# Kernel optimization log

Measured on AMD Instinct MI355X. Metric: run time of the kernel, lower is better.

## Reference

```python
import jax, jax.numpy as jnp
import numpy as np


def setup_inputs() -> dict:
    key = jax.random.key(0)
    k_x, k1, k2, k3 = jax.random.split(key, 4)
    dim, hidden, out_dim = 4096, 8192, 4096
    x = jax.random.normal(k_x, (4, 2048, dim), dtype=jnp.float32)
    # VNNILinear initializes weight = randn(out, in) * 0.02
    w1 = jax.random.normal(k1, (hidden, dim), dtype=jnp.float32) * 0.02
    w2 = jax.random.normal(k2, (out_dim, hidden), dtype=jnp.float32) * 0.02
    w3 = jax.random.normal(k3, (hidden, dim), dtype=jnp.float32) * 0.02
    return {"x": x, "w1": w1, "w2": w2, "w3": w3}


def _quant_linear(x, w):
    """Emulate VNNILinear int8 weight-quantized matmul (inference path).

    Per-output-channel symmetric quant: scale = max|w_row| / 127,
    w_q = round(w / scale) in int8, y = x @ (w_q * scale).T.
    """
    w_max = jnp.clip(jnp.max(jnp.abs(w), axis=1, keepdims=True), 1e-6)  # [out,1]
    scale_w = w_max / 127.0
    w_q = jnp.round(w / scale_w).astype(jnp.int8)
    w_dq = w_q.astype(jnp.float32) * scale_w  # dequantized weight
    return jnp.einsum('bsd,hd->bsh', x, w_dq)


def reference(x, w1, w2, w3):
    # SwiGLU: w2( silu(w1(x)) * w3(x) ), all bias-free, int8 VNNI weight quant
    h = jax.nn.silu(_quant_linear(x, w1)) * _quant_linear(x, w3)  # [B,S,hidden]
    return _quant_linear(h, w2)  # [B,S,out_dim]
```

## Files before the change

### kernel.cpp

```cpp
#include <hip/hip_runtime.h>
#include <hip/hip_bf16.h>
#include <stdint.h>


typedef short bf16x8 __attribute__((ext_vector_type(8)));
typedef float f32x4  __attribute__((ext_vector_type(4)));
typedef float f32x16 __attribute__((ext_vector_type(16)));
typedef int   i32x4  __attribute__((ext_vector_type(4)));
typedef int   i32x16 __attribute__((ext_vector_type(16)));

__device__ __forceinline__ unsigned short f2bf(float f) {
  unsigned u = __builtin_bit_cast(unsigned, f);
  u += 0x7FFFu + ((u >> 16) & 1u);
  return (unsigned short)(u >> 16);
}

#define GLOAD_LDS16(gaddr, laddr)                                             \
  __builtin_amdgcn_global_load_lds(                                           \
      (const __attribute__((address_space(1))) void*)(gaddr),                 \
      (__attribute__((address_space(3))) void*)(laddr), 16, 0, 0)

#define FENCE()      asm volatile("" ::: "memory")
#define BAR()        __builtin_amdgcn_s_barrier()
#define WAIT_LGKM(n) asm volatile("s_waitcnt lgkmcnt(" #n ")" ::: "memory")
#define WAIT_VM8()   asm volatile("s_waitcnt vmcnt(8)" ::: "memory")
#define WAIT_VM4()   asm volatile("s_waitcnt vmcnt(4)" ::: "memory")
#define WAIT_VM0()   asm volatile("s_waitcnt vmcnt(0)" ::: "memory")
#define SFENCE()     __builtin_amdgcn_sched_barrier(0)
#define PRIO1()      __builtin_amdgcn_s_setprio(1)
#define PRIO0()      __builtin_amdgcn_s_setprio(0)


template <int NCH>
__global__ void quant_rows_i8_sp(const float* __restrict__ w,
                                 char* __restrict__ q,
                                 float* __restrict__ scale, float clip) {
  const int cols = NCH * 1024;
  const float* wr = w + (size_t)blockIdx.x * cols;
  char* qr = q + (size_t)blockIdx.x * cols;

  float4 v[NCH];
  float m = 0.f;
#pragma unroll
  for (int j = 0; j < NCH; ++j) {
    v[j] = *reinterpret_cast<const float4*>(wr + threadIdx.x * 4 + j * 1024);
    m = fmaxf(m, fmaxf(fmaxf(fabsf(v[j].x), fabsf(v[j].y)),
                       fmaxf(fabsf(v[j].z), fabsf(v[j].w))));
  }
#pragma unroll
  for (int off = 32; off; off >>= 1) m = fmaxf(m, __shfl_xor(m, off));
  __shared__ float smax[4];
  if ((threadIdx.x & 63) == 0) smax[threadIdx.x >> 6] = m;
  __syncthreads();
  m = fmaxf(fmaxf(smax[0], smax[1]), fmaxf(smax[2], smax[3]));

  const float s = fmaxf(m, clip) / 127.0f;
  if (threadIdx.x == 0) scale[blockIdx.x] = s;
#pragma unroll
  for (int j = 0; j < NCH; ++j) {
    int b0 = (int)rintf(v[j].x / s), b1 = (int)rintf(v[j].y / s);
    int b2 = (int)rintf(v[j].z / s), b3 = (int)rintf(v[j].w / s);
    unsigned pk = (b0 & 0xff) | ((b1 & 0xff) << 8) | ((b2 & 0xff) << 16)
                  | ((b3 & 0xff) << 24);
    *reinterpret_cast<unsigned*>(qr + threadIdx.x * 4 + j * 1024) = pk;
  }
}

template <int NCH>
__global__ void quant_rows_bf16_sp(const float* __restrict__ w,
                                   unsigned short* __restrict__ wq) {
  const int cols = NCH * 1024;
  const float* wr = w + (size_t)blockIdx.x * cols;
  unsigned short* wqr = wq + (size_t)blockIdx.x * cols;

  float4 v[NCH];
  float m = 0.f;
#pragma unroll
  for (int j = 0; j < NCH; ++j) {
    v[j] = *reinterpret_cast<const float4*>(wr + threadIdx.x * 4 + j * 1024);
    m = fmaxf(m, fmaxf(fmaxf(fabsf(v[j].x), fabsf(v[j].y)),
                       fmaxf(fabsf(v[j].z), fabsf(v[j].w))));
  }
#pragma unroll
  for (int off = 32; off; off >>= 1) m = fmaxf(m, __shfl_xor(m, off));
  __shared__ float smax[4];
  if ((threadIdx.x & 63) == 0) smax[threadIdx.x >> 6] = m;
  __syncthreads();
  m = fmaxf(fmaxf(smax[0], smax[1]), fmaxf(smax[2], smax[3]));

  const float s = fmaxf(m, 1e-6f) / 127.0f;
#pragma unroll
  for (int j = 0; j < NCH; ++j) {
    ushort4 o;
    o.x = f2bf(rintf(v[j].x / s) * s);
    o.y = f2bf(rintf(v[j].y / s) * s);
    o.z = f2bf(rintf(v[j].z / s) * s);
    o.w = f2bf(rintf(v[j].w / s) * s);
    *reinterpret_cast<ushort4*>(wqr + threadIdx.x * 4 + j * 1024) = o;
  }
}


__device__ __forceinline__ void xcd_swizzle(int& bx, int& by, int gx, int gy) {
  int nwg = gx * gy;
  int bid = by * gx + bx;
  int cpx = nwg >> 3;
  int s = (bid & 7) * cpx + (bid >> 3);
  by = s / gx;
  bx = s % gx;
}

__global__ __launch_bounds__(512, 2)
void gemm_i8_swiglu_kernel(const char* __restrict__ Aq,
                           const char* __restrict__ B1q,
                           const char* __restrict__ B3q,
                           const float* __restrict__ sx,
                           const float* __restrict__ sw1,
                           const float* __restrict__ sw3,
                           unsigned short* __restrict__ H,
                           int M, int N, int K) {
  __shared__ alignas(1024) char lds[131072];

  int bx = blockIdx.x, by = blockIdx.y;
  xcd_swizzle(bx, by, gridDim.x, gridDim.y);
  const int brow = by * 256, bcol = bx * 128;

  const int t = threadIdx.x, lane = t & 63, w = t >> 6;
  const int wr = w >> 2, wc = w & 3;
  const int l31 = lane & 31, hi = lane >> 5;
  const bool wodd = (w & 1);
  const int NT = K >> 6;

  const int rS = t >> 2;
  const int gcS = ((t & 3) ^ ((t >> 3) & 3)) * 16;
  const char* srcA  = Aq  + (size_t)(brow + rS) * K + gcS;
  const char* srcB1 = B1q + (size_t)(bcol + rS) * K + gcS;
  const char* srcB3 = B3q + (size_t)(bcol + rS) * K + gcS;

#define STAGE_P1(pA_, pB1_, pB3_, sp, ko)                                     \
  if (!wodd) {                                                                \
    GLOAD_LDS16((pA_) + (ko), (sp) + t * 16);                                 \
    GLOAD_LDS16((pA_) + (size_t)128 * K + (ko), (sp) + 8192 + t * 16);        \
  } else {                                                                    \
    GLOAD_LDS16((pB1_) + (ko), (sp) + 16384 + t * 16);                        \
    GLOAD_LDS16((pB3_) + (ko), (sp) + 24576 + t * 16);                        \
  }
#define STAGE_P2(pA_, pB1_, pB3_, sp, ko)                                     \
  if (wodd) {                                                                 \
    GLOAD_LDS16((pA_) + (ko), (sp) + t * 16);                                 \
    GLOAD_LDS16((pA_) + (size_t)128 * K + (ko), (sp) + 8192 + t * 16);        \
  } else {                                                                    \
    GLOAD_LDS16((pB1_) + (ko), (sp) + 16384 + t * 16);                        \
    GLOAD_LDS16((pB3_) + (ko), (sp) + 24576 + t * 16);                        \
  }

  STAGE_P1(srcA, srcB1, srcB3, lds, 0);
  STAGE_P2(srcA, srcB1, srcB3, lds, 0);
  STAGE_P1(srcA, srcB1, srcB3, lds + 32768, (size_t)64);
  STAGE_P2(srcA, srcB1, srcB3, lds + 32768, (size_t)64);
  STAGE_P1(srcA, srcB1, srcB3, lds + 65536, (size_t)128);
  STAGE_P2(srcA, srcB1, srcB3, lds + 65536, (size_t)128);
  WAIT_VM8();
  FENCE(); BAR();

  const int sx2 = (l31 >> 1) & 3;
  const int aoff  = (wr * 128 + l31) * 64 + ((hi ^ sx2) * 16);
  const int boff1 = 16384 + (wc * 32 + l31) * 64 + ((hi ^ sx2) * 16);
  const int boff3 = boff1 + 8192;
  const int kx0 = wodd ? 32 : 0;
  const int kx1 = kx0 ^ 32;

  i32x16 acc[4][2] = {};
  i32x4 a0[4], b10, b30;
  i32x4 a1[4], b11, b31;

#pragma unroll
  for (int m = 0; m < 4; ++m)
    a0[m] = *reinterpret_cast<const i32x4*>(lds + (aoff ^ kx0) + m * 2048);
  b10 = *reinterpret_cast<const i32x4*>(lds + (boff1 ^ kx0));
  b30 = *reinterpret_cast<const i32x4*>(lds + (boff3 ^ kx0));

#define MFMA8(ar, b1r, b3r)                                                   \
  acc[0][0] = __builtin_amdgcn_mfma_i32_32x32x32_i8(ar[0], b1r, acc[0][0], 0, 0, 0); \
  acc[0][1] = __builtin_amdgcn_mfma_i32_32x32x32_i8(ar[0], b3r, acc[0][1], 0, 0, 0); \
  acc[1][0] = __builtin_amdgcn_mfma_i32_32x32x32_i8(ar[1], b1r, acc[1][0], 0, 0, 0); \
  acc[1][1] = __builtin_amdgcn_mfma_i32_32x32x32_i8(ar[1], b3r, acc[1][1], 0, 0, 0); \
  acc[2][0] = __builtin_amdgcn_mfma_i32_32x32x32_i8(ar[2], b1r, acc[2][0], 0, 0, 0); \
  acc[2][1] = __builtin_amdgcn_mfma_i32_32x32x32_i8(ar[2], b3r, acc[2][1], 0, 0, 0); \
  acc[3][0] = __builtin_amdgcn_mfma_i32_32x32x32_i8(ar[3], b1r, acc[3][0], 0, 0, 0); \
  acc[3][1] = __builtin_amdgcn_mfma_i32_32x32x32_i8(ar[3], b3r, acc[3][1], 0, 0, 0)

  int kb = 0;
  for (; kb < NT - 4; kb += 4) {
    const char* pA  = srcA  + (size_t)kb * 64;
    const char* pB1 = srcB1 + (size_t)kb * 64;
    const char* pB3 = srcB3 + (size_t)kb * 64;
#pragma unroll
    for (int s = 0; s < 4; ++s) {
      const char* sl = lds + s * 32768;
      const char* sn = lds + (((s + 1) & 3) * 32768);
      char* sp = lds + (((s + 3) & 3) * 32768);
      const int ko = (s + 3) * 64;

      a1[0] = *reinterpret_cast<const i32x4*>(sl + (aoff ^ kx1));
      a1[1] = *reinterpret_cast<const i32x4*>(sl + (aoff ^ kx1) + 2048);
      a1[2] = *reinterpret_cast<const i32x4*>(sl + (aoff ^ kx1) + 4096);
      a1[3] = *reinterpret_cast<const i32x4*>(sl + (aoff ^ kx1) + 6144);
      b11 = *reinterpret_cast<const i32x4*>(sl + (boff1 ^ kx1));
      b31 = *reinterpret_cast<const i32x4*>(sl + (boff3 ^ kx1));
      STAGE_P1(pA, pB1, pB3, sp, ko);
      WAIT_LGKM(6); SFENCE();
      PRIO1(); MFMA8(a0, b10, b30); PRIO0();

      STAGE_P2(pA, pB1, pB3, sp, ko);
      WAIT_VM8();
      WAIT_LGKM(0);
      FENCE(); BAR();
      a0[0] = *reinterpret_cast<const i32x4*>(sn + (aoff ^ kx0));
      a0[1] = *reinterpret_cast<const i32x4*>(sn + (aoff ^ kx0) + 2048);
      a0[2] = *reinterpret_cast<const i32x4*>(sn + (aoff ^ kx0) + 4096);
      a0[3] = *reinterpret_cast<const i32x4*>(sn + (aoff ^ kx0) + 6144);
      b10 = *reinterpret_cast<const i32x4*>(sn + (boff1 ^ kx0));
      b30 = *reinterpret_cast<const i32x4*>(sn + (boff3 ^ kx0));
      SFENCE();
      PRIO1(); MFMA8(a1, b11, b31); PRIO0();
    }
  }

  for (int k = kb; k < NT; ++k) {
    const char* sl = lds + (k & 3) * 32768;
    const bool pf = (k + 3 < NT);

    a1[0] = *reinterpret_cast<const i32x4*>(sl + (aoff ^ kx1));
    a1[1] = *reinterpret_cast<const i32x4*>(sl + (aoff ^ kx1) + 2048);
    a1[2] = *reinterpret_cast<const i32x4*>(sl + (aoff ^ kx1) + 4096);
    a1[3] = *reinterpret_cast<const i32x4*>(sl + (aoff ^ kx1) + 6144);
    b11 = *reinterpret_cast<const i32x4*>(sl + (boff1 ^ kx1));
    b31 = *reinterpret_cast<const i32x4*>(sl + (boff3 ^ kx1));
    if (pf) {
      char* sp = lds + (((k + 3) & 3) * 32768);
      STAGE_P1(srcA, srcB1, srcB3, sp, (size_t)(k + 3) * 64);
    }
    WAIT_LGKM(6); SFENCE();
    PRIO1(); MFMA8(a0, b10, b30); PRIO0();

    if (pf) {
      char* sp = lds + (((k + 3) & 3) * 32768);
      STAGE_P2(srcA, srcB1, srcB3, sp, (size_t)(k + 3) * 64);
      WAIT_VM8();
    } else if (k == NT - 3) {
      WAIT_VM4();
    } else if (k == NT - 2) {
      WAIT_VM0();
    }
    WAIT_LGKM(0);
    FENCE(); BAR();
    if (k + 1 < NT) {
      const char* sn = lds + ((k + 1) & 3) * 32768;
      a0[0] = *reinterpret_cast<const i32x4*>(sn + (aoff ^ kx0));
      a0[1] = *reinterpret_cast<const i32x4*>(sn + (aoff ^ kx0) + 2048);
      a0[2] = *reinterpret_cast<const i32x4*>(sn + (aoff ^ kx0) + 4096);
      a0[3] = *reinterpret_cast<const i32x4*>(sn + (aoff ^ kx0) + 6144);
      b10 = *reinterpret_cast<const i32x4*>(sn + (boff1 ^ kx0));
      b30 = *reinterpret_cast<const i32x4*>(sn + (boff3 ^ kx0));
    }
    SFENCE();
    PRIO1(); MFMA8(a1, b11, b31); PRIO0();
  }
#undef MFMA8
#undef STAGE_P1
#undef STAGE_P2

  const int ocol = bcol + wc * 32 + l31;
  const int rowb = brow + wr * 128 + 4 * hi;
  const float sw1c = sw1[ocol], sw3c = sw3[ocol];
#pragma unroll
  for (int m = 0; m < 4; ++m) {
#pragma unroll
    for (int rq = 0; rq < 4; ++rq) {
      const int r0 = rowb + m * 32 + 8 * rq;
      const f32x4 sx4 = *reinterpret_cast<const f32x4*>(sx + r0);
#pragma unroll
      for (int j = 0; j < 4; ++j) {
        float y1 = (float)acc[m][0][rq * 4 + j] * (sx4[j] * sw1c);
        float y3 = (float)acc[m][1][rq * 4 + j] * (sx4[j] * sw3c);
        float hv = (y1 / (1.f + __expf(-y1))) * y3;
        H[(size_t)(r0 + j) * N + ocol] = f2bf(hv);
      }
    }
  }
}

__global__ __launch_bounds__(512, 2)
void gemm_bf16_kernel(const unsigned short* __restrict__ A,
                      const unsigned short* __restrict__ B,
                      float* __restrict__ C, int M, int N, int K) {
  __shared__ alignas(1024) unsigned short lds[65536];

  int bx = blockIdx.x, by = blockIdx.y;
  xcd_swizzle(bx, by, gridDim.x, gridDim.y);
  const int brow = by * 256, bcol = bx * 256;

  const int t = threadIdx.x, lane = t & 63, w = t >> 6;
  const int wr = w >> 2, wc = w & 3;
  const int l31 = lane & 31, hi = lane >> 5;
  const bool wodd = (w & 1);
  const int NT = K >> 5;

  const int rS = t >> 2;
  const int cS = ((t & 3) ^ ((t >> 3) & 3)) * 8;
  const unsigned short* srcA = A + (size_t)(brow + rS) * K + cS;
  const unsigned short* srcB = B + (size_t)(bcol + rS) * K + cS;

#define STAGE_P1(pA_, pB_, sp, ko)                                            \
  if (!wodd) {                                                                \
    GLOAD_LDS16((pA_) + (ko), (sp) + t * 8);                                  \
    GLOAD_LDS16((pA_) + (size_t)128 * K + (ko), (sp) + 4096 + t * 8);         \
  } else {                                                                    \
    GLOAD_LDS16((pB_) + (ko), (sp) + 8192 + t * 8);                           \
    GLOAD_LDS16((pB_) + (size_t)128 * K + (ko), (sp) + 12288 + t * 8);        \
  }
#define STAGE_P2(pA_, pB_, sp, ko)                                            \
  if (wodd) {                                                                 \
    GLOAD_LDS16((pA_) + (ko), (sp) + t * 8);                                  \
    GLOAD_LDS16((pA_) + (size_t)128 * K + (ko), (sp) + 4096 + t * 8);         \
  } else {                                                                    \
    GLOAD_LDS16((pB_) + (ko), (sp) + 8192 + t * 8);                           \
    GLOAD_LDS16((pB_) + (size_t)128 * K + (ko), (sp) + 12288 + t * 8);        \
  }

  STAGE_P1(srcA, srcB, lds, 0);
  STAGE_P2(srcA, srcB, lds, 0);
  STAGE_P1(srcA, srcB, lds + 16384, (size_t)32);
  STAGE_P2(srcA, srcB, lds + 16384, (size_t)32);
  STAGE_P1(srcA, srcB, lds + 32768, (size_t)64);
  STAGE_P2(srcA, srcB, lds + 32768, (size_t)64);
  WAIT_VM8();
  FENCE(); BAR();

  const int sx2 = (l31 >> 1) & 3;
  const int aoff  = (wr * 128 + l31) * 32 + ((hi ^ sx2) * 8);
  const int boff0 = 8192 + (wc * 64 + l31) * 32 + ((hi ^ sx2) * 8);
  const int boff1b = boff0 + 1024;
  const int kx0 = wodd ? 16 : 0;
  const int kx1 = kx0 ^ 16;

  f32x16 acc[4][2] = {};
  bf16x8 a0[4], b00, b01;
  bf16x8 a1[4], b10, b11;

#pragma unroll
  for (int m = 0; m < 4; ++m)
    a0[m] = *reinterpret_cast<const bf16x8*>(&lds[(aoff ^ kx0) + m * 1024]);
  b00 = *reinterpret_cast<const bf16x8*>(&lds[boff0 ^ kx0]);
  b01 = *reinterpret_cast<const bf16x8*>(&lds[boff1b ^ kx0]);

#define MFMA8(ar, bx0, bx1)                                                   \
  acc[0][0] = __builtin_amdgcn_mfma_f32_32x32x16_bf16(ar[0], bx0, acc[0][0], 0, 0, 0); \
  acc[0][1] = __builtin_amdgcn_mfma_f32_32x32x16_bf16(ar[0], bx1, acc[0][1], 0, 0, 0); \
  acc[1][0] = __builtin_amdgcn_mfma_f32_32x32x16_bf16(ar[1], bx0, acc[1][0], 0, 0, 0); \
  acc[1][1] = __builtin_amdgcn_mfma_f32_32x32x16_bf16(ar[1], bx1, acc[1][1], 0, 0, 0); \
  acc[2][0] = __builtin_amdgcn_mfma_f32_32x32x16_bf16(ar[2], bx0, acc[2][0], 0, 0, 0); \
  acc[2][1] = __builtin_amdgcn_mfma_f32_32x32x16_bf16(ar[2], bx1, acc[2][1], 0, 0, 0); \
  acc[3][0] = __builtin_amdgcn_mfma_f32_32x32x16_bf16(ar[3], bx0, acc[3][0], 0, 0, 0); \
  acc[3][1] = __builtin_amdgcn_mfma_f32_32x32x16_bf16(ar[3], bx1, acc[3][1], 0, 0, 0)

  int kb = 0;
  for (; kb < NT - 4; kb += 4) {
    const unsigned short* pA = srcA + (size_t)kb * 32;
    const unsigned short* pB = srcB + (size_t)kb * 32;
#pragma unroll
    for (int s = 0; s < 4; ++s) {
      const unsigned short* sl = lds + s * 16384;
      const unsigned short* sn = lds + (((s + 1) & 3) * 16384);
      unsigned short* sp = lds + (((s + 3) & 3) * 16384);
      const int ko = (s + 3) * 32;

      a1[0] = *reinterpret_cast<const bf16x8*>(sl + (aoff ^ kx1));
      a1[1] = *reinterpret_cast<const bf16x8*>(sl + (aoff ^ kx1) + 1024);
      a1[2] = *reinterpret_cast<const bf16x8*>(sl + (aoff ^ kx1) + 2048);
      a1[3] = *reinterpret_cast<const bf16x8*>(sl + (aoff ^ kx1) + 3072);
      b10 = *reinterpret_cast<const bf16x8*>(sl + (boff0 ^ kx1));
      b11 = *reinterpret_cast<const bf16x8*>(sl + (boff1b ^ kx1));
      STAGE_P1(pA, pB, sp, ko);
      WAIT_LGKM(6); SFENCE();
      PRIO1(); MFMA8(a0, b00, b01); PRIO0();

      STAGE_P2(pA, pB, sp, ko);
      WAIT_VM8();
      WAIT_LGKM(0);
      FENCE(); BAR();
      a0[0] = *reinterpret_cast<const bf16x8*>(sn + (aoff ^ kx0));
      a0[1] = *reinterpret_cast<const bf16x8*>(sn + (aoff ^ kx0) + 1024);
      a0[2] = *reinterpret_cast<const bf16x8*>(sn + (aoff ^ kx0) + 2048);
      a0[3] = *reinterpret_cast<const bf16x8*>(sn + (aoff ^ kx0) + 3072);
      b00 = *reinterpret_cast<const bf16x8*>(sn + (boff0 ^ kx0));
      b01 = *reinterpret_cast<const bf16x8*>(sn + (boff1b ^ kx0));
      SFENCE();
      PRIO1(); MFMA8(a1, b10, b11); PRIO0();
    }
  }

  for (int k = kb; k < NT; ++k) {
    const unsigned short* sl = &lds[(k & 3) * 16384];
    const bool pf = (k + 3 < NT);

    a1[0] = *reinterpret_cast<const bf16x8*>(sl + (aoff ^ kx1));
    a1[1] = *reinterpret_cast<const bf16x8*>(sl + (aoff ^ kx1) + 1024);
    a1[2] = *reinterpret_cast<const bf16x8*>(sl + (aoff ^ kx1) + 2048);
    a1[3] = *reinterpret_cast<const bf16x8*>(sl + (aoff ^ kx1) + 3072);
    b10 = *reinterpret_cast<const bf16x8*>(sl + (boff0 ^ kx1));
    b11 = *reinterpret_cast<const bf16x8*>(sl + (boff1b ^ kx1));
    if (pf) {
      unsigned short* sp = lds + (((k + 3) & 3) * 16384);
      STAGE_P1(srcA, srcB, sp, (size_t)(k + 3) * 32);
    }
    WAIT_LGKM(6); SFENCE();
    PRIO1(); MFMA8(a0, b00, b01); PRIO0();

    if (pf) {
      unsigned short* sp = lds + (((k + 3) & 3) * 16384);
      STAGE_P2(srcA, srcB, sp, (size_t)(k + 3) * 32);
      WAIT_VM8();
    } else if (k == NT - 3) {
      WAIT_VM4();
    } else if (k == NT - 2) {
      WAIT_VM0();
    }
    WAIT_LGKM(0);
    FENCE(); BAR();
    if (k + 1 < NT) {
      const unsigned short* sn = &lds[((k + 1) & 3) * 16384];
      a0[0] = *reinterpret_cast<const bf16x8*>(sn + (aoff ^ kx0));
      a0[1] = *reinterpret_cast<const bf16x8*>(sn + (aoff ^ kx0) + 1024);
      a0[2] = *reinterpret_cast<const bf16x8*>(sn + (aoff ^ kx0) + 2048);
      a0[3] = *reinterpret_cast<const bf16x8*>(sn + (aoff ^ kx0) + 3072);
      b00 = *reinterpret_cast<const bf16x8*>(sn + (boff0 ^ kx0));
      b01 = *reinterpret_cast<const bf16x8*>(sn + (boff1b ^ kx0));
    }
    SFENCE();
    PRIO1(); MFMA8(a1, b10, b11); PRIO0();
  }
#undef MFMA8
#undef STAGE_P1
#undef STAGE_P2

  const int ocol = bcol + wc * 64 + l31;
  const int rowb = brow + wr * 128 + 4 * hi;
#pragma unroll
  for (int m = 0; m < 4; ++m)
#pragma unroll
    for (int n = 0; n < 2; ++n)
#pragma unroll
      for (int rq = 0; rq < 4; ++rq)
#pragma unroll
        for (int j = 0; j < 4; ++j)
          C[(size_t)(rowb + m * 32 + 8 * rq + j) * N + (ocol + n * 32)] =
              acc[m][n][rq * 4 + j];
}


extern "C" void kernel_launch(void* const* d_in, const int* in_sizes, int n_in,
                              void* d_out, int out_size, void* d_ws,
                              size_t ws_size, hipStream_t stream) {
  const float* x  = (const float*)d_in[0];
  const float* w1 = (const float*)d_in[1];
  const float* w2 = (const float*)d_in[2];
  const float* w3 = (const float*)d_in[3];
  float* out = (float*)d_out;

  const int DIM = 4096, HID = 8192;
  const int M = in_sizes[0] / DIM;

  char* xq  = (char*)d_ws;
  char* w1q = xq + (size_t)M * DIM;
  char* w3q = w1q + (size_t)HID * DIM;
  unsigned short* w2b = (unsigned short*)(w3q + (size_t)HID * DIM);
  unsigned short* h = w2b + (size_t)DIM * HID;
  float* sx  = (float*)(h + (size_t)M * HID);
  float* sw1 = sx + M;
  float* sw3 = sw1 + HID;

  quant_rows_i8_sp<4><<<HID, 256, 0, stream>>>(w1, w1q, sw1, 1e-6f);
  quant_rows_i8_sp<4><<<HID, 256, 0, stream>>>(w3, w3q, sw3, 1e-6f);
  quant_rows_i8_sp<4><<<M, 256, 0, stream>>>(x, xq, sx, 1e-30f);
  quant_rows_bf16_sp<8><<<DIM, 256, 0, stream>>>(w2, w2b);

  gemm_i8_swiglu_kernel<<<dim3(HID / 128, M / 256), 512, 0, stream>>>(
      xq, w1q, w3q, sx, sw1, sw3, h, M, HID, DIM);
  gemm_bf16_kernel<<<dim3(DIM / 256, M / 256), 512, 0, stream>>>(
      h, w2b, out, M, DIM, HID);
}
```

Measured before the change: 1.217 ms.

## Shrink int8 SwiGLU GEMM tile to 128 rows with 3-stage pipeline for higher occupancy

Halves the M tile of the int8 SwiGLU GEMM from 256 to 128 rows and cuts the LDS ring from four 32KB stages to three 24KB stages, so more workgroups can fit per CU (launch bounds raised to 4). The staging is simplified so every wave loads A and both B tiles rather than alternating halves between odd and even waves, and per-wave accumulators drop from 8 to 4 MFMA tiles. This aims to improve latency hiding through occupancy, at the cost of lower arithmetic intensity per tile, more redundant B traffic, and a shallower prefetch depth.

Result: slower. 1.314 ms (+8.0%).

```diff
diff --git a/kernel.cpp b/kernel.cpp
--- a/kernel.cpp
+++ b/kernel.cpp
@@ -25,6 +25,7 @@
 #define WAIT_LGKM(n) asm volatile("s_waitcnt lgkmcnt(" #n ")" ::: "memory")
 #define WAIT_VM8()   asm volatile("s_waitcnt vmcnt(8)" ::: "memory")
 #define WAIT_VM4()   asm volatile("s_waitcnt vmcnt(4)" ::: "memory")
+#define WAIT_VM3()   asm volatile("s_waitcnt vmcnt(3)" ::: "memory")
 #define WAIT_VM0()   asm volatile("s_waitcnt vmcnt(0)" ::: "memory")
 #define SFENCE()     __builtin_amdgcn_sched_barrier(0)
 #define PRIO1()      __builtin_amdgcn_s_setprio(1)
@@ -110,7 +111,7 @@
   bx = s % gx;
 }
 
-__global__ __launch_bounds__(512, 2)
+__global__ __launch_bounds__(512, 4)
 void gemm_i8_swiglu_kernel(const char* __restrict__ Aq,
                            const char* __restrict__ B1q,
                            const char* __restrict__ B3q,
@@ -119,16 +120,15 @@
                            const float* __restrict__ sw3,
                            unsigned short* __restrict__ H,
                            int M, int N, int K) {
-  __shared__ alignas(1024) char lds[131072];
+  __shared__ alignas(1024) char lds[73728];
 
   int bx = blockIdx.x, by = blockIdx.y;
   xcd_swizzle(bx, by, gridDim.x, gridDim.y);
-  const int brow = by * 256, bcol = bx * 128;
+  const int brow = by * 128, bcol = bx * 128;
 
   const int t = threadIdx.x, lane = t & 63, w = t >> 6;
   const int wr = w >> 2, wc = w & 3;
   const int l31 = lane & 31, hi = lane >> 5;
-  const bool wodd = (w & 1);
   const int NT = K >> 6;
 
   const int rS = t >> 2;
@@ -137,145 +137,78 @@
   const char* srcB1 = B1q + (size_t)(bcol + rS) * K + gcS;
   const char* srcB3 = B3q + (size_t)(bcol + rS) * K + gcS;
 
-#define STAGE_P1(pA_, pB1_, pB3_, sp, ko)                                     \
-  if (!wodd) {                                                                \
-    GLOAD_LDS16((pA_) + (ko), (sp) + t * 16);                                 \
-    GLOAD_LDS16((pA_) + (size_t)128 * K + (ko), (sp) + 8192 + t * 16);        \
-  } else {                                                                    \
-    GLOAD_LDS16((pB1_) + (ko), (sp) + 16384 + t * 16);                        \
-    GLOAD_LDS16((pB3_) + (ko), (sp) + 24576 + t * 16);                        \
-  }
-#define STAGE_P2(pA_, pB1_, pB3_, sp, ko)                                     \
-  if (wodd) {                                                                 \
-    GLOAD_LDS16((pA_) + (ko), (sp) + t * 16);                                 \
-    GLOAD_LDS16((pA_) + (size_t)128 * K + (ko), (sp) + 8192 + t * 16);        \
-  } else {                                                                    \
-    GLOAD_LDS16((pB1_) + (ko), (sp) + 16384 + t * 16);                        \
-    GLOAD_LDS16((pB3_) + (ko), (sp) + 24576 + t * 16);                        \
-  }
-
-  STAGE_P1(srcA, srcB1, srcB3, lds, 0);
-  STAGE_P2(srcA, srcB1, srcB3, lds, 0);
-  STAGE_P1(srcA, srcB1, srcB3, lds + 32768, (size_t)64);
-  STAGE_P2(srcA, srcB1, srcB3, lds + 32768, (size_t)64);
-  STAGE_P1(srcA, srcB1, srcB3, lds + 65536, (size_t)128);
-  STAGE_P2(srcA, srcB1, srcB3, lds + 65536, (size_t)128);
-  WAIT_VM8();
+#define STAGE_A(soff, kt)                                                     \
+  GLOAD_LDS16(srcA + (size_t)(kt) * 64, lds + (soff) + t * 16);
+#define STAGE_B(soff, kt)                                                     \
+  GLOAD_LDS16(srcB1 + (size_t)(kt) * 64, lds + (soff) + 8192 + t * 16);       \
+  GLOAD_LDS16(srcB3 + (size_t)(kt) * 64, lds + (soff) + 16384 + t * 16);
+
+  STAGE_A(0, 0); STAGE_B(0, 0);
+  STAGE_A(24576, 1); STAGE_B(24576, 1);
+  WAIT_VM3();
   FENCE(); BAR();
 
   const int sx2 = (l31 >> 1) & 3;
-  const int aoff  = (wr * 128 + l31) * 64 + ((hi ^ sx2) * 16);
-  const int boff1 = 16384 + (wc * 32 + l31) * 64 + ((hi ^ sx2) * 16);
+  const int aoff  = (wr * 64 + l31) * 64 + ((hi ^ sx2) * 16);
+  const int boff1 = 8192 + (wc * 32 + l31) * 64 + ((hi ^ sx2) * 16);
   const int boff3 = boff1 + 8192;
-  const int kx0 = wodd ? 32 : 0;
-  const int kx1 = kx0 ^ 32;
-
-  i32x16 acc[4][2] = {};
-  i32x4 a0[4], b10, b30;
-  i32x4 a1[4], b11, b31;
-
-#pragma unroll
-  for (int m = 0; m < 4; ++m)
-    a0[m] = *reinterpret_cast<const i32x4*>(lds + (aoff ^ kx0) + m * 2048);
-  b10 = *reinterpret_cast<const i32x4*>(lds + (boff1 ^ kx0));
-  b30 = *reinterpret_cast<const i32x4*>(lds + (boff3 ^ kx0));
-
-#define MFMA8(ar, b1r, b3r)                                                   \
+
+  i32x16 acc[2][2] = {};
+  i32x4 a0[2], b10, b30;
+  i32x4 a1[2], b11, b31;
+
+  a0[0] = *reinterpret_cast<const i32x4*>(lds + aoff);
+  a0[1] = *reinterpret_cast<const i32x4*>(lds + aoff + 2048);
+  b10 = *reinterpret_cast<const i32x4*>(lds + boff1);
+  b30 = *reinterpret_cast<const i32x4*>(lds + boff3);
+
+#define MFMA4(ar, b1r, b3r)                                                   \
   acc[0][0] = __builtin_amdgcn_mfma_i32_32x32x32_i8(ar[0], b1r, acc[0][0], 0, 0, 0); \
   acc[0][1] = __builtin_amdgcn_mfma_i32_32x32x32_i8(ar[0], b3r, acc[0][1], 0, 0, 0); \
   acc[1][0] = __builtin_amdgcn_mfma_i32_32x32x32_i8(ar[1], b1r, acc[1][0], 0, 0, 0); \
-  acc[1][1] = __builtin_amdgcn_mfma_i32_32x32x32_i8(ar[1], b3r, acc[1][1], 0, 0, 0); \
-  acc[2][0] = __builtin_amdgcn_mfma_i32_32x32x32_i8(ar[2], b1r, acc[2][0], 0, 0, 0); \
-  acc[2][1] = __builtin_amdgcn_mfma_i32_32x32x32_i8(ar[2], b3r, acc[2][1], 0, 0, 0); \
-  acc[3][0] = __builtin_amdgcn_mfma_i32_32x32x32_i8(ar[3], b1r, acc[3][0], 0, 0, 0); \
-  acc[3][1] = __builtin_amdgcn_mfma_i32_32x32x32_i8(ar[3], b3r, acc[3][1], 0, 0, 0)
-
-  int kb = 0;
-  for (; kb < NT - 4; kb += 4) {
-    const char* pA  = srcA  + (size_t)kb * 64;
-    const char* pB1 = srcB1 + (size_t)kb * 64;
-    const char* pB3 = srcB3 + (size_t)kb * 64;
-#pragma unroll
-    for (int s = 0; s < 4; ++s) {
-      const char* sl = lds + s * 32768;
-      const char* sn = lds + (((s + 1) & 3) * 32768);
-      char* sp = lds + (((s + 3) & 3) * 32768);
-      const int ko = (s + 3) * 64;
-
-      a1[0] = *reinterpret_cast<const i32x4*>(sl + (aoff ^ kx1));
-      a1[1] = *reinterpret_cast<const i32x4*>(sl + (aoff ^ kx1) + 2048);
-      a1[2] = *reinterpret_cast<const i32x4*>(sl + (aoff ^ kx1) + 4096);
-      a1[3] = *reinterpret_cast<const i32x4*>(sl + (aoff ^ kx1) + 6144);
-      b11 = *reinterpret_cast<const i32x4*>(sl + (boff1 ^ kx1));
-      b31 = *reinterpret_cast<const i32x4*>(sl + (boff3 ^ kx1));
-      STAGE_P1(pA, pB1, pB3, sp, ko);
-      WAIT_LGKM(6); SFENCE();
-      PRIO1(); MFMA8(a0, b10, b30); PRIO0();
-
-      STAGE_P2(pA, pB1, pB3, sp, ko);
-      WAIT_VM8();
-      WAIT_LGKM(0);
-      FENCE(); BAR();
-      a0[0] = *reinterpret_cast<const i32x4*>(sn + (aoff ^ kx0));
-      a0[1] = *reinterpret_cast<const i32x4*>(sn + (aoff ^ kx0) + 2048);
-      a0[2] = *reinterpret_cast<const i32x4*>(sn + (aoff ^ kx0) + 4096);
-      a0[3] = *reinterpret_cast<const i32x4*>(sn + (aoff ^ kx0) + 6144);
-      b10 = *reinterpret_cast<const i32x4*>(sn + (boff1 ^ kx0));
-      b30 = *reinterpret_cast<const i32x4*>(sn + (boff3 ^ kx0));
-      SFENCE();
-      PRIO1(); MFMA8(a1, b11, b31); PRIO0();
-    }
-  }
-
-  for (int k = kb; k < NT; ++k) {
-    const char* sl = lds + (k & 3) * 32768;
-    const bool pf = (k + 3 < NT);
-
-    a1[0] = *reinterpret_cast<const i32x4*>(sl + (aoff ^ kx1));
-    a1[1] = *reinterpret_cast<const i32x4*>(sl + (aoff ^ kx1) + 2048);
-    a1[2] = *reinterpret_cast<const i32x4*>(sl + (aoff ^ kx1) + 4096);
-    a1[3] = *reinterpret_cast<const i32x4*>(sl + (aoff ^ kx1) + 6144);
-    b11 = *reinterpret_cast<const i32x4*>(sl + (boff1 ^ kx1));
-    b31 = *reinterpret_cast<const i32x4*>(sl + (boff3 ^ kx1));
+  acc[1][1] = __builtin_amdgcn_mfma_i32_32x32x32_i8(ar[1], b3r, acc[1][1], 0, 0, 0)
+
+  int sl = 0, sn = 24576, sp = 49152;
+
+  for (int k = 0; k < NT; ++k) {
+    const bool pf = (k + 2 < NT);
+
+    a1[0] = *reinterpret_cast<const i32x4*>(lds + sl + (aoff ^ 32));
+    a1[1] = *reinterpret_cast<const i32x4*>(lds + sl + (aoff ^ 32) + 2048);
+    b11 = *reinterpret_cast<const i32x4*>(lds + sl + (boff1 ^ 32));
+    b31 = *reinterpret_cast<const i32x4*>(lds + sl + (boff3 ^ 32));
+    if (pf) { STAGE_A(sp, k + 2); }
+    WAIT_LGKM(4); SFENCE();
+    PRIO1(); MFMA4(a0, b10, b30); PRIO0();
+
     if (pf) {
-      char* sp = lds + (((k + 3) & 3) * 32768);
-      STAGE_P1(srcA, srcB1, srcB3, sp, (size_t)(k + 3) * 64);
-    }
-    WAIT_LGKM(6); SFENCE();
-    PRIO1(); MFMA8(a0, b10, b30); PRIO0();
-
-    if (pf) {
-      char* sp = lds + (((k + 3) & 3) * 32768);
-      STAGE_P2(srcA, srcB1, srcB3, sp, (size_t)(k + 3) * 64);
-      WAIT_VM8();
-    } else if (k == NT - 3) {
-      WAIT_VM4();
+      STAGE_B(sp, k + 2);
+      WAIT_VM3();
     } else if (k == NT - 2) {
       WAIT_VM0();
     }
     WAIT_LGKM(0);
     FENCE(); BAR();
     if (k + 1 < NT) {
-      const char* sn = lds + ((k + 1) & 3) * 32768;
-      a0[0] = *reinterpret_cast<const i32x4*>(sn + (aoff ^ kx0));
-      a0[1] = *reinterpret_cast<const i32x4*>(sn + (aoff ^ kx0) + 2048);
-      a0[2] = *reinterpret_cast<const i32x4*>(sn + (aoff ^ kx0) + 4096);
-      a0[3] = *reinterpret_cast<const i32x4*>(sn + (aoff ^ kx0) + 6144);
-      b10 = *reinterpret_cast<const i32x4*>(sn + (boff1 ^ kx0));
-      b30 = *reinterpret_cast<const i32x4*>(sn + (boff3 ^ kx0));
+      a0[0] = *reinterpret_cast<const i32x4*>(lds + sn + aoff);
+      a0[1] = *reinterpret_cast<const i32x4*>(lds + sn + aoff + 2048);
+      b10 = *reinterpret_cast<const i32x4*>(lds + sn + boff1);
+      b30 = *reinterpret_cast<const i32x4*>(lds + sn + boff3);
     }
     SFENCE();
-    PRIO1(); MFMA8(a1, b11, b31); PRIO0();
-  }
-#undef MFMA8
-#undef STAGE_P1
-#undef STAGE_P2
+    PRIO1(); MFMA4(a1, b11, b31); PRIO0();
+
+    int tmp = sl; sl = sn; sn = sp; sp = tmp;
+  }
+#undef MFMA4
+#undef STAGE_A
+#undef STAGE_B
 
   const int ocol = bcol + wc * 32 + l31;
-  const int rowb = brow + wr * 128 + 4 * hi;
+  const int rowb = brow + wr * 64 + 4 * hi;
   const float sw1c = sw1[ocol], sw3c = sw3[ocol];
 #pragma unroll
-  for (int m = 0; m < 4; ++m) {
+  for (int m = 0; m < 2; ++m) {
 #pragma unroll
     for (int rq = 0; rq < 4; ++rq) {
       const int r0 = rowb + m * 32 + 8 * rq;
@@ -486,7 +419,7 @@
   quant_rows_i8_sp<4><<<M, 256, 0, stream>>>(x, xq, sx, 1e-30f);
   quant_rows_bf16_sp<8><<<DIM, 256, 0, stream>>>(w2, w2b);
 
-  gemm_i8_swiglu_kernel<<<dim3(HID / 128, M / 256), 512, 0, stream>>>(
+  gemm_i8_swiglu_kernel<<<dim3(HID / 128, M / 128), 512, 0, stream>>>(
       xq, w1q, w3q, sx, sw1, sw3, h, M, HID, DIM);
   gemm_bf16_kernel<<<dim3(DIM / 256, M / 256), 512, 0, stream>>>(
       h, w2b, out, M, DIM, HID);
```
